# Performance work log

Measured on AMD Instinct MI355X. Metric: run time of the kernel, lower is better.

## Reference

```python
import jax, jax.numpy as jnp
import numpy as np

N = 100000   # nodes
E = 1600000  # edges (no self loops; module adds them)
D = 128      # in_dim == out_dim
BN_EPS = 1e-5
NORM_EPS = 1e-12


def setup_inputs() -> dict:
    key = jax.random.key(0)
    ks = jax.random.split(key, 9)
    x = jax.random.normal(ks[0], (N, D), jnp.float32)
    src = jax.random.randint(ks[1], (E,), 0, N, dtype=jnp.int32)
    dst = jax.random.randint(ks[2], (E,), 0, N, dtype=jnp.int32)
    dst = jnp.where(dst == src, (dst + 1) % N, dst)  # no pre-existing self loops
    edge_index = jnp.stack([src, dst], axis=0)
    edge_w = jax.random.uniform(ks[3], (E, 2), jnp.float32)
    # MySAGEConv.linear: Linear(2*D -> D) since concat=True
    W_lin = jax.random.normal(ks[4], (2 * D, D), jnp.float32) * (1.0 / np.sqrt(2 * D))
    b_lin = jnp.zeros((D,), jnp.float32)
    # BatchNorm1d(D)
    gamma = jnp.ones((D,), jnp.float32)
    beta = jnp.zeros((D,), jnp.float32)
    # PositionEmbedding(2, D): Linear(2->D//2, no bias), ReLU, Linear(D//2->D, no bias)
    pos_w1 = jax.random.normal(ks[5], (2, D // 2), jnp.float32) * 0.1
    pos_w2 = jax.random.normal(ks[6], (D // 2, D), jnp.float32) * 0.1
    return {"x": x, "edge_index": edge_index, "edge_w": edge_w,
            "W_lin": W_lin, "b_lin": b_lin, "gamma": gamma, "beta": beta,
            "pos_w1": pos_w1, "pos_w2": pos_w2}


def reference(x, edge_index, edge_w, W_lin, b_lin, gamma, beta, pos_w1, pos_w2):
    src, dst = edge_index[0], edge_index[1]
    # Position embedding is computed by the block but DISCARDED inside MySAGEConv.forward,
    # because add_remaining_self_loops(edge_index, None, 1, N) overwrites edge_weight with None.
    _pe = jnp.maximum(edge_w @ pos_w1, 0.0) @ pos_w2  # [E, D], unused (faithful to bug)
    # add_remaining_self_loops: append a self loop for every node
    loops = jnp.arange(N, dtype=src.dtype)
    src_f = jnp.concatenate([src, loops])
    dst_f = jnp.concatenate([dst, loops])
    # message = x_j (edge_weight is None); aggr = 'mean' scatter over destinations
    msg = x[src_f]                                           # [E+N, D] gather
    summed = jax.ops.segment_sum(msg, dst_f, num_segments=N)  # [N, D] scatter-add
    cnt = jax.ops.segment_sum(jnp.ones((E + N, 1), x.dtype), dst_f, num_segments=N)
    aggr = summed / cnt                                      # every node has >=1 (self loop)
    # update: concat + linear + L2 normalize
    h = jnp.concatenate([x, aggr], axis=-1) @ W_lin + b_lin   # [N, D]
    h = h / jnp.maximum(jnp.linalg.norm(h, axis=-1, keepdims=True), NORM_EPS)
    # BatchNorm1d (training-mode batch stats, biased variance)
    mu = jnp.mean(h, axis=0)
    var = jnp.var(h, axis=0)
    h = (h - mu) * jax.lax.rsqrt(var + BN_EPS) * gamma + beta
    # residual (in_dim == out_dim) + ReLU
    return jnp.maximum(h + x, 0.0)
```

## Files before the change

kernel.cpp:

```cpp
#include <hip/hip_runtime.h>
#include <hip/hip_bf16.h>

typedef __attribute__((ext_vector_type(4))) float f32x4;
typedef __attribute__((ext_vector_type(8))) short short8;
typedef unsigned short u16;
typedef unsigned long long u64;

static __device__ __forceinline__ u16 f2bf(float f) {
    __hip_bfloat16 h = __float2bfloat16(f);
    return __builtin_bit_cast(u16, h);
}
static __device__ __forceinline__ float bf2f(u16 u) {
    unsigned int w = ((unsigned int)u) << 16;
    return __builtin_bit_cast(float, w);
}

__global__ void k_pre(const float* __restrict__ x, u16* __restrict__ xb, int total8,
                      const int* __restrict__ dst, int* __restrict__ deg,
                      int E, int chunk, int cvtBlocks) {
    int tid = threadIdx.x;
    if ((int)blockIdx.x < cvtBlocks) {
        const float4* x4 = (const float4*)x;
        int stride = cvtBlocks * 256;
        for (int i = blockIdx.x * 256 + tid; i < total8; i += stride) {
            float4 a = x4[i * 2], b = x4[i * 2 + 1];
            union { u16 u[8]; short8 v; } o;
            o.u[0] = f2bf(a.x); o.u[1] = f2bf(a.y); o.u[2] = f2bf(a.z); o.u[3] = f2bf(a.w);
            o.u[4] = f2bf(b.x); o.u[5] = f2bf(b.y); o.u[6] = f2bf(b.z); o.u[7] = f2bf(b.w);
            *(short8*)(xb + (size_t)i * 8) = o.v;
        }
    } else {
        int group = blockIdx.x & 7;
        int bseq = (blockIdx.x - cvtBlocks) >> 3;
        int nblk = (gridDim.x - cvtBlocks) >> 3;
        int lo = group * chunk, hi = lo + chunk;
        int E4 = E >> 2;
        const int4* d4 = (const int4*)dst;
        int stride = nblk * 256;
        int gid = bseq * 256 + tid;
        for (int i = gid; i < E4; i += stride) {
            int4 v = d4[i];
            if (v.x >= lo && v.x < hi) atomicAdd(&deg[v.x], 1);
            if (v.y >= lo && v.y < hi) atomicAdd(&deg[v.y], 1);
            if (v.z >= lo && v.z < hi) atomicAdd(&deg[v.z], 1);
            if (v.w >= lo && v.w < hi) atomicAdd(&deg[v.w], 1);
        }
        if (group == 0) {
            for (int e = E4 * 4 + gid; e < E; e += stride)
                atomicAdd(&deg[dst[e]], 1);
        }
    }
}

__global__ void k_scan_a(const int* __restrict__ deg, int* __restrict__ bsum, int n) {
    __shared__ int s[256];
    int tid = threadIdx.x;
    int i = blockIdx.x * 256 + tid;
    s[tid] = (i < n) ? deg[i] : 0;
    __syncthreads();
    for (int ofs = 128; ofs > 0; ofs >>= 1) {
        if (tid < ofs) s[tid] += s[tid + ofs];
        __syncthreads();
    }
    if (tid == 0) bsum[blockIdx.x] = s[0];
}

__global__ void k_scan_b(const int* __restrict__ bsum, int* __restrict__ boff, int nb,
                         int* __restrict__ offN) {
    __shared__ int s[512];
    int tid = threadIdx.x;
    int v = (tid < nb) ? bsum[tid] : 0;
    s[tid] = v;
    __syncthreads();
    for (int ofs = 1; ofs < 512; ofs <<= 1) {
        int t = (tid >= ofs) ? s[tid - ofs] : 0;
        __syncthreads();
        s[tid] += t;
        __syncthreads();
    }
    if (tid < nb) boff[tid] = s[tid] - v;
    if (tid == nb - 1) offN[0] = s[tid];
}

__global__ void k_scan_c(const int* __restrict__ deg, const int* __restrict__ boff,
                         int* __restrict__ off, int* __restrict__ cur, int n) {
    __shared__ int s[256];
    int tid = threadIdx.x;
    int i = blockIdx.x * 256 + tid;
    int v = (i < n) ? deg[i] : 0;
    s[tid] = v;
    __syncthreads();
    for (int ofs = 1; ofs < 256; ofs <<= 1) {
        int t = (tid >= ofs) ? s[tid - ofs] : 0;
        __syncthreads();
        s[tid] += t;
        __syncthreads();
    }
    int excl = s[tid] - v + boff[blockIdx.x];
    if (i < n) { off[i] = excl; cur[i] = excl; }
}

__global__ void k_fill(const int* __restrict__ src, const int* __restrict__ dst,
                       int* __restrict__ cur, int* __restrict__ csr, int E, int chunk) {
    const int NX = 8;
    int group = blockIdx.x & (NX - 1);
    int bseq = blockIdx.x >> 3;
    int nblk = gridDim.x >> 3;
    int lo = group * chunk, hi = lo + chunk;
    int E4 = E >> 2;
    const int4* d4 = (const int4*)dst;
    int stride = nblk * blockDim.x;
    int gid = bseq * blockDim.x + threadIdx.x;
    for (int i = gid; i < E4; i += stride) {
        int4 v = d4[i];
        int e = i * 4;
        if (v.x >= lo && v.x < hi) { int p = atomicAdd(&cur[v.x], 1); csr[p] = src[e]; }
        if (v.y >= lo && v.y < hi) { int p = atomicAdd(&cur[v.y], 1); csr[p] = src[e + 1]; }
        if (v.z >= lo && v.z < hi) { int p = atomicAdd(&cur[v.z], 1); csr[p] = src[e + 2]; }
        if (v.w >= lo && v.w < hi) { int p = atomicAdd(&cur[v.w], 1); csr[p] = src[e + 3]; }
    }
    if (group == 0) {
        for (int e = E4 * 4 + gid; e < E; e += stride) {
            int d = dst[e];
            int p = atomicAdd(&cur[d], 1);
            csr[p] = src[e];
        }
    }
}

__global__ void k_aggr(const u16* __restrict__ xb, const int* __restrict__ off,
                       const int* __restrict__ csr, u16* __restrict__ aggr, int n) {
    int node = (blockIdx.x * blockDim.x + threadIdx.x) >> 6;
    if (node >= n) return;
    int lane = threadIdx.x & 63;
    int c = lane & 15;
    int j = lane >> 4;
    const short8* x8 = (const short8*)xb;
    int s0 = off[node], s1 = off[node + 1];
    float acc[8] = {0.f, 0.f, 0.f, 0.f, 0.f, 0.f, 0.f, 0.f};
    int e = s0;
    for (; e + 16 <= s1; e += 16) {
        int r0 = csr[e + j], r1 = csr[e + j + 4], r2 = csr[e + j + 8], r3 = csr[e + j + 12];
        short8 v0 = x8[(size_t)r0 * 16 + c];
        short8 v1 = x8[(size_t)r1 * 16 + c];
        short8 v2 = x8[(size_t)r2 * 16 + c];
        short8 v3 = x8[(size_t)r3 * 16 + c];
#pragma unroll
        for (int i = 0; i < 8; ++i)
            acc[i] += (bf2f((u16)v0[i]) + bf2f((u16)v1[i])) +
                      (bf2f((u16)v2[i]) + bf2f((u16)v3[i]));
    }
    for (int r = e + j; r < s1; r += 4) {
        short8 v = x8[(size_t)csr[r] * 16 + c];
#pragma unroll
        for (int i = 0; i < 8; ++i) acc[i] += bf2f((u16)v[i]);
    }
#pragma unroll
    for (int i = 0; i < 8; ++i) {
        acc[i] += __shfl_xor(acc[i], 16, 64);
        acc[i] += __shfl_xor(acc[i], 32, 64);
    }
    if (j == 0) {
        short8 sv = x8[(size_t)node * 16 + c];
        float inv = 1.0f / (float)(s1 - s0 + 1);
        short8 o;
#pragma unroll
        for (int i = 0; i < 8; ++i)
            o[i] = (short)f2bf((acc[i] + bf2f((u16)sv[i])) * inv);
        *(short8*)(aggr + (size_t)node * 128 + c * 8) = o;
    }
}

__global__ __launch_bounds__(512, 2) void k_linear(
    const float* __restrict__ x, const u16* __restrict__ aggr,
    const float* __restrict__ W, const float* __restrict__ b_lin,
    u16* __restrict__ hout ,
    float* __restrict__ ssp, float* __restrict__ bnsum, float* __restrict__ bnsq,
    int n, int ntiles, int npad) {
    __shared__ u16 WT[32768];
    int tid = threadIdx.x;

    {
        int col = tid & 127;
        int kq0 = tid >> 7;
        int mask = (col & 15) << 3;
        char* base = (char*)WT + col * 512;
#pragma unroll
        for (int i = 0; i < 16; ++i) {
            int kq = kq0 + i * 4;
            int k = kq * 4;
            float w0 = W[(size_t)(k + 0) * 128 + col];
            float w1 = W[(size_t)(k + 1) * 128 + col];
            float w2 = W[(size_t)(k + 2) * 128 + col];
            float w3 = W[(size_t)(k + 3) * 128 + col];
            u64 q = (u64)f2bf(w0) | ((u64)f2bf(w1) << 16) |
                    ((u64)f2bf(w2) << 32) | ((u64)f2bf(w3) << 48);
            *(u64*)(base + ((8 * kq) ^ mask)) = q;
        }
    }
    __syncthreads();

    int wave = tid >> 6, l = tid & 63, lr = l & 15, lg = l >> 4;
    int pair = wave >> 1, hf = wave & 1;

    short8 breg[4][8];
#pragma unroll
    for (int ct2 = 0; ct2 < 4; ++ct2) {
        int col = hf * 64 + ct2 * 16 + lr;
        const char* rowp = (const char*)WT + col * 512;
        int mask = (col & 15) << 3;
#pragma unroll
        for (int kk = 0; kk < 8; ++kk) {
            int kb = kk * 64 + 8 * lg;
            u64 lo = *(const u64*)(rowp + (kb ^ mask));
            u64 hi = *(const u64*)(rowp + ((kb + 32) ^ mask));
            union { u64 q[2]; short8 v; } bu;
            bu.q[0] = lo; bu.q[1] = hi;
            breg[ct2][kk] = bu.v;
        }
    }

    int stride4 = gridDim.x * 4;

    for (int base = blockIdx.x * 4; base < ntiles; base += stride4) {
        int tile = base + pair;
        bool active = tile < ntiles;
        int rowA = tile * 16 + lr;
        bool rv = active && rowA < n;

        float4 xa[4], xc[4];
        ushort4 ua[4], ub[4];
#pragma unroll
        for (int kk = 0; kk < 4; ++kk) {
            int k1 = kk * 32 + 4 * lg;
            xa[kk] = rv ? *(const float4*)(x + (size_t)rowA * 128 + k1)
                        : make_float4(0.f, 0.f, 0.f, 0.f);
            xc[kk] = rv ? *(const float4*)(x + (size_t)rowA * 128 + k1 + 16)
                        : make_float4(0.f, 0.f, 0.f, 0.f);
        }
#pragma unroll
        for (int kk = 0; kk < 4; ++kk) {
            const u16* ap = aggr + (size_t)rowA * 128 + kk * 32 + 4 * lg;
            ua[kk] = rv ? *(const ushort4*)ap : make_ushort4(0, 0, 0, 0);
            ub[kk] = rv ? *(const ushort4*)(ap + 16) : make_ushort4(0, 0, 0, 0);
        }

        short8 av[8];
#pragma unroll
        for (int kk = 0; kk < 4; ++kk) {
            av[kk][0] = (short)f2bf(xa[kk].x); av[kk][1] = (short)f2bf(xa[kk].y);
            av[kk][2] = (short)f2bf(xa[kk].z); av[kk][3] = (short)f2bf(xa[kk].w);
            av[kk][4] = (short)f2bf(xc[kk].x); av[kk][5] = (short)f2bf(xc[kk].y);
            av[kk][6] = (short)f2bf(xc[kk].z); av[kk][7] = (short)f2bf(xc[kk].w);
            av[kk + 4][0] = (short)ua[kk].x; av[kk + 4][1] = (short)ua[kk].y;
            av[kk + 4][2] = (short)ua[kk].z; av[kk + 4][3] = (short)ua[kk].w;
            av[kk + 4][4] = (short)ub[kk].x; av[kk + 4][5] = (short)ub[kk].y;
            av[kk + 4][6] = (short)ub[kk].z; av[kk + 4][7] = (short)ub[kk].w;
        }

        f32x4 acc[4];
#pragma unroll
        for (int ct2 = 0; ct2 < 4; ++ct2) acc[ct2] = (f32x4){0.f, 0.f, 0.f, 0.f};
#pragma unroll
        for (int kk = 0; kk < 8; ++kk)
#pragma unroll
            for (int ct2 = 0; ct2 < 4; ++ct2)
                acc[ct2] = __builtin_amdgcn_mfma_f32_16x16x32_bf16(av[kk], breg[ct2][kk],
                                                                   acc[ct2], 0, 0, 0);

        float ss[4] = {0.f, 0.f, 0.f, 0.f};
#pragma unroll
        for (int ct2 = 0; ct2 < 4; ++ct2) {
            float bl = b_lin[hf * 64 + ct2 * 16 + lr];
#pragma unroll
            for (int q = 0; q < 4; ++q) {
                acc[ct2][q] += bl;
                ss[q] += acc[ct2][q] * acc[ct2][q];
            }
        }
#pragma unroll
        for (int m = 1; m < 16; m <<= 1) {
#pragma unroll
            for (int q = 0; q < 4; ++q) ss[q] += __shfl_xor(ss[q], m, 64);
        }
        if (active) {
            int rq0 = tile * 16 + 4 * lg;
            if (lr == 0)
                *(float4*)&ssp[hf * npad + rq0] = make_float4(ss[0], ss[1], ss[2], ss[3]);
            u16* hp = hout + (size_t)tile * 4096 + 2048;
#pragma unroll
            for (int ct2 = 0; ct2 < 4; ++ct2) {
                ushort4 o;
                o.x = f2bf(acc[ct2][0]); o.y = f2bf(acc[ct2][1]);
                o.z = f2bf(acc[ct2][2]); o.w = f2bf(acc[ct2][3]);
                *(ushort4*)(hp + (hf * 4 + ct2) * 256 + l * 4) = o;
            }
        }
    }

    __syncthreads();

    float s1a[4] = {0, 0, 0, 0};
    float s2a[4] = {0, 0, 0, 0};
    for (int base = blockIdx.x * 4; base < ntiles; base += stride4) {
        int tile = base + pair;
        if (tile >= ntiles) continue;
        int rq0 = tile * 16 + 4 * lg;
        float rn[4];
#pragma unroll
        for (int q = 0; q < 4; ++q) {
            float s2 = ssp[rq0 + q] + ssp[npad + rq0 + q];
            rn[q] = 1.0f / fmaxf(sqrtf(s2), 1e-12f);
        }
        const u16* hp = hout + (size_t)tile * 4096 + 2048;
#pragma unroll
        for (int ct2 = 0; ct2 < 4; ++ct2) {
            ushort4 hv = *(const ushort4*)(hp + (hf * 4 + ct2) * 256 + l * 4);
            float p1 = 0.f, p2 = 0.f;
            float h0 = bf2f(hv.x) * rn[0], h1 = bf2f(hv.y) * rn[1];
            float h2 = bf2f(hv.z) * rn[2], h3 = bf2f(hv.w) * rn[3];
            if (rq0 + 0 < n) { p1 += h0; p2 += h0 * h0; }
            if (rq0 + 1 < n) { p1 += h1; p2 += h1 * h1; }
            if (rq0 + 2 < n) { p1 += h2; p2 += h2 * h2; }
            if (rq0 + 3 < n) { p1 += h3; p2 += h3 * h3; }
            s1a[ct2] += p1; s2a[ct2] += p2;
        }
    }

#pragma unroll
    for (int ct2 = 0; ct2 < 4; ++ct2) {
        float v1 = s1a[ct2], v2 = s2a[ct2];
        v1 += __shfl_xor(v1, 16, 64); v1 += __shfl_xor(v1, 32, 64);
        v2 += __shfl_xor(v2, 16, 64); v2 += __shfl_xor(v2, 32, 64);
        if (lg == 0) {
            atomicAdd(&bnsum[hf * 64 + ct2 * 16 + lr], v1);
            atomicAdd(&bnsq[hf * 64 + ct2 * 16 + lr], v2);
        }
    }
}

__global__ __launch_bounds__(512) void k_final(
    const float* __restrict__ ssp, const float* __restrict__ x,
    const float* __restrict__ bnsum, const float* __restrict__ bnsq,
    const float* __restrict__ gamma, const float* __restrict__ beta,
    float* __restrict__ out, float invN, int n, int npad) {
    __shared__ float cf[256];
    __shared__ float ot[16 * 132];
    int tid = threadIdx.x;
    int tile = blockIdx.x;
    if (tid < 128) {
        float mu = bnsum[tid] * invN;
        float var = bnsq[tid] * invN - mu * mu;
        float a = gamma[tid] * rsqrtf(var + 1e-5f);
        cf[tid] = a;
        cf[128 + tid] = beta[tid] - mu * a;
    }
    __syncthreads();

    {
        const u16* hp = (const u16*)out + (size_t)tile * 4096 + 2048;
        int ct = tid >> 6, l = tid & 63;
        ushort4 hv = *(const ushort4*)(hp + ct * 256 + l * 4);
        int col = ct * 16 + (l & 15);
        float a = cf[col], b = cf[128 + col];
        int rl0 = 4 * (l >> 4);
        int rq0 = tile * 16 + rl0;
        float rn0 = 1.0f / fmaxf(sqrtf(ssp[rq0 + 0] + ssp[npad + rq0 + 0]), 1e-12f);
        float rn1 = 1.0f / fmaxf(sqrtf(ssp[rq0 + 1] + ssp[npad + rq0 + 1]), 1e-12f);
        float rn2 = 1.0f / fmaxf(sqrtf(ssp[rq0 + 2] + ssp[npad + rq0 + 2]), 1e-12f);
        float rn3 = 1.0f / fmaxf(sqrtf(ssp[rq0 + 3] + ssp[npad + rq0 + 3]), 1e-12f);
        ot[(rl0 + 0) * 132 + col] = bf2f(hv.x) * rn0 * a + b;
        ot[(rl0 + 1) * 132 + col] = bf2f(hv.y) * rn1 * a + b;
        ot[(rl0 + 2) * 132 + col] = bf2f(hv.z) * rn2 * a + b;
        ot[(rl0 + 3) * 132 + col] = bf2f(hv.w) * rn3 * a + b;
    }
    __syncthreads();

    {
        int rl = tid >> 5, c4 = tid & 31;
        int row = tile * 16 + rl;
        if (row < n) {
            float4 xv = *(const float4*)(x + (size_t)row * 128 + c4 * 4);
            const float* op = &ot[rl * 132 + c4 * 4];
            float4 o;
            o.x = fmaxf(op[0] + xv.x, 0.f);
            o.y = fmaxf(op[1] + xv.y, 0.f);
            o.z = fmaxf(op[2] + xv.z, 0.f);
            o.w = fmaxf(op[3] + xv.w, 0.f);
            *(float4*)(out + (size_t)row * 128 + c4 * 4) = o;
        }
    }
}

extern "C" void kernel_launch(void* const* d_in, const int* in_sizes, int n_in,
                              void* d_out, int out_size, void* d_ws, size_t ws_size,
                              hipStream_t stream) {
    const float* x     = (const float*)d_in[0];
    const int*   ei    = (const int*)d_in[1];
    const float* W     = (const float*)d_in[3];
    const float* b_lin = (const float*)d_in[4];
    const float* gamma = (const float*)d_in[5];
    const float* beta  = (const float*)d_in[6];
    int N = in_sizes[0] / 128;
    int E = in_sizes[1] / 2;
    const int* src = ei;
    const int* dst = ei + E;

    int ntiles = (N + 15) / 16;
    int npad = ntiles * 16;

    char* p = (char*)d_ws;
    auto alloc = [&](size_t bytes) { char* r = p; p += (bytes + 255) & ~(size_t)255; return r; };
    int*   deg   = (int*)alloc((size_t)N * 4);
    float* bnsum = (float*)alloc(128 * 4);
    float* bnsq  = (float*)alloc(128 * 4);
    size_t zspan = (char*)(bnsq + 128) - (char*)deg;
    int*   off   = (int*)alloc((size_t)(N + 1) * 4);
    int*   cur   = (int*)alloc((size_t)N * 4);
    int*   csr   = (int*)alloc((size_t)E * 4);
    int*   bsum  = (int*)alloc(512 * 4);
    int*   boff  = (int*)alloc(512 * 4);
    float* ssp   = (float*)alloc((size_t)npad * 2 * 4);
    u16*   aggr  = (u16*)alloc((size_t)N * 128 * 2);

    u16* xbf = (u16*)d_out;

    hipMemsetAsync(deg, 0, zspan, stream);

    const int NGROUP = 8;
    int chunk = (N + NGROUP - 1) / NGROUP;
    const int CVTB = 768;

    k_pre<<<CVTB + 1024, 256, 0, stream>>>(x, xbf, N * 16, dst, deg, E, chunk, CVTB);
    int nb = (N + 255) / 256;
    k_scan_a<<<nb, 256, 0, stream>>>(deg, bsum, N);
    k_scan_b<<<1, 512, 0, stream>>>(bsum, boff, nb, off + N);
    k_scan_c<<<nb, 256, 0, stream>>>(deg, boff, off, cur, N);
    k_fill<<<1024, 256, 0, stream>>>(src, dst, cur, csr, E, chunk);
    k_aggr<<<(int)(((size_t)N * 64 + 255) / 256), 256, 0, stream>>>(xbf, off, csr, aggr, N);
    k_linear<<<256, 512, 0, stream>>>(x, aggr, W, b_lin, (u16*)d_out, ssp,
                                      bnsum, bnsq, N, ntiles, npad);
    k_final<<<ntiles, 512, 0, stream>>>(ssp, x, bnsum, bnsq, gamma, beta,
                                        (float*)d_out, 1.0f / (float)N, N, npad);
}
```

Measured before the change: 297.3 us.

## Build CSR via per-slice LDS histograms instead of global atomics

Degree counting now uses per-block shared-memory histograms over edge slices, writing per-slice partial counts into a scratch buffer that aliases the aggregation buffer. The scan kernel turns these slice counts into per-slice prefix offsets. The fill kernel then places edges using those offsets plus LDS atomics, so the global cursor array and its contended global atomics go away. In exchange there is extra traffic for the 64×N partial-count array and a column-wise scan over it. The LDS histogram size is hard-coded and only fits node chunks up to 12544.

```diff
diff --git a/kernel.cpp b/kernel.cpp
--- a/kernel.cpp
+++ b/kernel.cpp
@@ -6,6 +6,9 @@
 typedef unsigned short u16;
 typedef unsigned long long u64;
 
+#define NSLICE 64
+#define LDSN 12544
+
 static __device__ __forceinline__ u16 f2bf(float f) {
     __hip_bfloat16 h = __float2bfloat16(f);
     return __builtin_bit_cast(u16, h);
@@ -16,8 +19,9 @@
 }
 
 __global__ void k_pre(const float* __restrict__ x, u16* __restrict__ xb, int total8,
-                      const int* __restrict__ dst, int* __restrict__ deg,
-                      int E, int chunk, int cvtBlocks) {
+                      const int* __restrict__ dst, int* __restrict__ part,
+                      int E, int chunk, int n, int cvtBlocks, int sl4) {
+    __shared__ int lh[LDSN];
     int tid = threadIdx.x;
     if ((int)blockIdx.x < cvtBlocks) {
         const float4* x4 = (const float4*)x;
@@ -30,39 +34,61 @@
             *(short8*)(xb + (size_t)i * 8) = o.v;
         }
     } else {
-        int group = blockIdx.x & 7;
-        int bseq = (blockIdx.x - cvtBlocks) >> 3;
-        int nblk = (gridDim.x - cvtBlocks) >> 3;
-        int lo = group * chunk, hi = lo + chunk;
+        int b = blockIdx.x - cvtBlocks;
+        int g = b & 7;
+        int s = b >> 3;
+        int lo = g * chunk;
+        int hi = min(lo + chunk, n);
+        int cnt = hi - lo;
+        for (int i = tid; i < cnt; i += 256) lh[i] = 0;
+        __syncthreads();
         int E4 = E >> 2;
         const int4* d4 = (const int4*)dst;
-        int stride = nblk * 256;
-        int gid = bseq * 256 + tid;
-        for (int i = gid; i < E4; i += stride) {
+        int i40 = s * sl4, i41 = min(i40 + sl4, E4);
+        for (int i = i40 + tid; i < i41; i += 256) {
             int4 v = d4[i];
-            if (v.x >= lo && v.x < hi) atomicAdd(&deg[v.x], 1);
-            if (v.y >= lo && v.y < hi) atomicAdd(&deg[v.y], 1);
-            if (v.z >= lo && v.z < hi) atomicAdd(&deg[v.z], 1);
-            if (v.w >= lo && v.w < hi) atomicAdd(&deg[v.w], 1);
-        }
-        if (group == 0) {
-            for (int e = E4 * 4 + gid; e < E; e += stride)
-                atomicAdd(&deg[dst[e]], 1);
-        }
-    }
-}
-
-__global__ void k_scan_a(const int* __restrict__ deg, int* __restrict__ bsum, int n) {
-    __shared__ int s[256];
+            if (v.x >= lo && v.x < hi) atomicAdd(&lh[v.x - lo], 1);
+            if (v.y >= lo && v.y < hi) atomicAdd(&lh[v.y - lo], 1);
+            if (v.z >= lo && v.z < hi) atomicAdd(&lh[v.z - lo], 1);
+            if (v.w >= lo && v.w < hi) atomicAdd(&lh[v.w - lo], 1);
+        }
+        if (s == NSLICE - 1) {
+            for (int e = E4 * 4 + tid; e < E; e += 256) {
+                int d = dst[e];
+                if (d >= lo && d < hi) atomicAdd(&lh[d - lo], 1);
+            }
+        }
+        __syncthreads();
+        int* pp = part + (size_t)s * n + lo;
+        for (int i = tid; i < cnt; i += 256) pp[i] = lh[i];
+    }
+}
+
+__global__ void k_scan_a(int* __restrict__ part, int* __restrict__ deg,
+                         int* __restrict__ bsum, int n) {
+    __shared__ int sm[256];
     int tid = threadIdx.x;
     int i = blockIdx.x * 256 + tid;
-    s[tid] = (i < n) ? deg[i] : 0;
+    int tot = 0;
+    if (i < n) {
+        int run = 0;
+#pragma unroll
+        for (int s = 0; s < NSLICE; ++s) {
+            size_t idx = (size_t)s * n + i;
+            int t = part[idx];
+            part[idx] = run;
+            run += t;
+        }
+        tot = run;
+        deg[i] = run;
+    }
+    sm[tid] = tot;
     __syncthreads();
     for (int ofs = 128; ofs > 0; ofs >>= 1) {
-        if (tid < ofs) s[tid] += s[tid + ofs];
-        __syncthreads();
-    }
-    if (tid == 0) bsum[blockIdx.x] = s[0];
+        if (tid < ofs) sm[tid] += sm[tid + ofs];
+        __syncthreads();
+    }
+    if (tid == 0) bsum[blockIdx.x] = sm[0];
 }
 
 __global__ void k_scan_b(const int* __restrict__ bsum, int* __restrict__ boff, int nb,
@@ -83,7 +109,7 @@
 }
 
 __global__ void k_scan_c(const int* __restrict__ deg, const int* __restrict__ boff,
-                         int* __restrict__ off, int* __restrict__ cur, int n) {
+                         int* __restrict__ off, int n) {
     __shared__ int s[256];
     int tid = threadIdx.x;
     int i = blockIdx.x * 256 + tid;
@@ -97,33 +123,53 @@
         __syncthreads();
     }
     int excl = s[tid] - v + boff[blockIdx.x];
-    if (i < n) { off[i] = excl; cur[i] = excl; }
+    if (i < n) off[i] = excl;
 }
 
 __global__ void k_fill(const int* __restrict__ src, const int* __restrict__ dst,
-                       int* __restrict__ cur, int* __restrict__ csr, int E, int chunk) {
-    const int NX = 8;
-    int group = blockIdx.x & (NX - 1);
-    int bseq = blockIdx.x >> 3;
-    int nblk = gridDim.x >> 3;
-    int lo = group * chunk, hi = lo + chunk;
+                       const int* __restrict__ off, const int* __restrict__ pre,
+                       int* __restrict__ csr, int E, int chunk, int n, int sl4) {
+    __shared__ int lcnt[LDSN];
+    int tid = threadIdx.x;
+    int g = blockIdx.x & 7;
+    int s = blockIdx.x >> 3;
+    int lo = g * chunk;
+    int hi = min(lo + chunk, n);
+    int cnt = hi - lo;
+    for (int i = tid; i < cnt; i += 256) lcnt[i] = 0;
+    __syncthreads();
     int E4 = E >> 2;
     const int4* d4 = (const int4*)dst;
-    int stride = nblk * blockDim.x;
-    int gid = bseq * blockDim.x + threadIdx.x;
-    for (int i = gid; i < E4; i += stride) {
+    const int4* s4 = (const int4*)src;
+    const int* prs = pre + (size_t)s * n;
+    int i40 = s * sl4, i41 = min(i40 + sl4, E4);
+    for (int i = i40 + tid; i < i41; i += 256) {
         int4 v = d4[i];
-        int e = i * 4;
-        if (v.x >= lo && v.x < hi) { int p = atomicAdd(&cur[v.x], 1); csr[p] = src[e]; }
-        if (v.y >= lo && v.y < hi) { int p = atomicAdd(&cur[v.y], 1); csr[p] = src[e + 1]; }
-        if (v.z >= lo && v.z < hi) { int p = atomicAdd(&cur[v.z], 1); csr[p] = src[e + 2]; }
-        if (v.w >= lo && v.w < hi) { int p = atomicAdd(&cur[v.w], 1); csr[p] = src[e + 3]; }
-    }
-    if (group == 0) {
-        for (int e = E4 * 4 + gid; e < E; e += stride) {
+        int4 u = s4[i];
+        if (v.x >= lo && v.x < hi) {
+            int p = off[v.x] + prs[v.x] + atomicAdd(&lcnt[v.x - lo], 1);
+            csr[p] = u.x;
+        }
+        if (v.y >= lo && v.y < hi) {
+            int p = off[v.y] + prs[v.y] + atomicAdd(&lcnt[v.y - lo], 1);
+            csr[p] = u.y;
+        }
+        if (v.z >= lo && v.z < hi) {
+            int p = off[v.z] + prs[v.z] + atomicAdd(&lcnt[v.z - lo], 1);
+            csr[p] = u.z;
+        }
+        if (v.w >= lo && v.w < hi) {
+            int p = off[v.w] + prs[v.w] + atomicAdd(&lcnt[v.w - lo], 1);
+            csr[p] = u.w;
+        }
+    }
+    if (s == NSLICE - 1) {
+        for (int e = E4 * 4 + tid; e < E; e += 256) {
             int d = dst[e];
-            int p = atomicAdd(&cur[d], 1);
-            csr[p] = src[e];
+            if (d >= lo && d < hi) {
+                int p = off[d] + prs[d] + atomicAdd(&lcnt[d - lo], 1);
+                csr[p] = src[e];
+            }
         }
     }
 }
@@ -414,29 +460,32 @@
     int*   deg   = (int*)alloc((size_t)N * 4);
     float* bnsum = (float*)alloc(128 * 4);
     float* bnsq  = (float*)alloc(128 * 4);
-    size_t zspan = (char*)(bnsq + 128) - (char*)deg;
+    size_t zoff  = (char*)bnsum - (char*)d_ws;
     int*   off   = (int*)alloc((size_t)(N + 1) * 4);
-    int*   cur   = (int*)alloc((size_t)N * 4);
     int*   csr   = (int*)alloc((size_t)E * 4);
     int*   bsum  = (int*)alloc(512 * 4);
     int*   boff  = (int*)alloc(512 * 4);
     float* ssp   = (float*)alloc((size_t)npad * 2 * 4);
     u16*   aggr  = (u16*)alloc((size_t)N * 128 * 2);
 
+    int* part = (int*)aggr;
+
     u16* xbf = (u16*)d_out;
 
-    hipMemsetAsync(deg, 0, zspan, stream);
-
-    const int NGROUP = 8;
-    int chunk = (N + NGROUP - 1) / NGROUP;
+    hipMemsetAsync((char*)d_ws + zoff, 0, 256 * 4, stream);
+
+    int chunk = (N + 7) / 8;
+    int E4 = E >> 2;
+    int sl4 = (E4 + NSLICE - 1) / NSLICE;
     const int CVTB = 768;
 
-    k_pre<<<CVTB + 1024, 256, 0, stream>>>(x, xbf, N * 16, dst, deg, E, chunk, CVTB);
+    k_pre<<<CVTB + 8 * NSLICE, 256, 0, stream>>>(x, xbf, N * 16, dst, part,
+                                                 E, chunk, N, CVTB, sl4);
     int nb = (N + 255) / 256;
-    k_scan_a<<<nb, 256, 0, stream>>>(deg, bsum, N);
+    k_scan_a<<<nb, 256, 0, stream>>>(part, deg, bsum, N);
     k_scan_b<<<1, 512, 0, stream>>>(bsum, boff, nb, off + N);
-    k_scan_c<<<nb, 256, 0, stream>>>(deg, boff, off, cur, N);
-    k_fill<<<1024, 256, 0, stream>>>(src, dst, cur, csr, E, chunk);
+    k_scan_c<<<nb, 256, 0, stream>>>(deg, boff, off, N);
+    k_fill<<<8 * NSLICE, 256, 0, stream>>>(src, dst, off, part, csr, E, chunk, N, sl4);
     k_aggr<<<(int)(((size_t)N * 64 + 255) / 256), 256, 0, stream>>>(xbf, off, csr, aggr, N);
     k_linear<<<256, 512, 0, stream>>>(x, aggr, W, b_lin, (u16*)d_out, ssp,
                                       bnsum, bnsq, N, ntiles, npad);
```

New measurement: 252.7 us. 1.18x faster.
